# Performance work log

Hardware: AMD Instinct MI355X
Metric: run time of the kernel (lower is better)

## Reference

```python
import jax, jax.numpy as jnp
import numpy as np

N = 100000
E = 6400000
DIMS = [34, 16, 16, 16, 4]


def setup_inputs() -> dict:
    key = jax.random.key(0)
    ks = jax.random.split(key, 12)
    x = jax.random.normal(ks[0], (N, DIMS[0]), dtype=jnp.float32)
    edge_index = jax.random.randint(ks[1], (2, E), 0, N, dtype=jnp.int64)
    inp = {"x": x, "edge_index": edge_index}
    for i in range(4):
        fan_in, fan_out = DIMS[i], DIMS[i + 1]
        s = (6.0 / (fan_in + fan_out)) ** 0.5  # glorot
        inp[f"W{i+1}"] = jax.random.uniform(ks[2 + 2 * i], (fan_in, fan_out), minval=-s, maxval=s, dtype=jnp.float32)
        inp[f"b{i+1}"] = jnp.zeros((fan_out,), dtype=jnp.float32)
    return inp


def gcn_layer(x, W, b, src, dst, norm):
    # x: [N, din] -> [N, dout]; PyG GCNConv: h = XW, aggregate norm*h[src] into dst, + bias
    h = x @ W
    msgs = h[src] * norm[:, None]                      # [E+N, dout]
    out = jax.ops.segment_sum(msgs, dst, num_segments=N)
    return out + b


def reference(x, edge_index, W1, b1, W2, b2, W3, b3, W4, b4):
    loop = jnp.arange(N, dtype=edge_index.dtype)
    src = jnp.concatenate([edge_index[0], loop])       # add self-loops
    dst = jnp.concatenate([edge_index[1], loop])
    deg = jax.ops.segment_sum(jnp.ones_like(dst, dtype=x.dtype), dst, num_segments=N)
    dinv = jnp.where(deg > 0, jax.lax.rsqrt(deg), 0.0)
    norm = dinv[src] * dinv[dst]                       # symmetric normalization per edge
    h = gcn_layer(x, W1, b1, src, dst, norm)
    h = jax.nn.relu(h)
    h = gcn_layer(h, W2, b2, src, dst, norm)
    h = jax.nn.relu(h)
    h = gcn_layer(h, W3, b3, src, dst, norm)
    h = jax.nn.relu(h)
    return gcn_layer(h, W4, b4, src, dst, norm)
```

## Files before the change

kernel.cpp:

```cpp
#include <hip/hip_runtime.h>
#include <hip/hip_bf16.h>


static constexpr int THREADS = 256;
static constexpr int BSHIFT  = 8;
static constexpr int NPB     = 256;
static constexpr int MAXB    = 512;
static constexpr int NCHUNK  = 512;
static constexpr int EPT     = 8;
static constexpr int SSHIFT  = 15;
static constexpr int NSHARD  = 4;


__global__ __launch_bounds__(THREADS)
void k_hist(const int* __restrict__ dst, int* __restrict__ hist_part,
            int e, int nbkt, int chunk) {
    __shared__ int h[MAXB];
    for (int t = threadIdx.x; t < nbkt; t += THREADS) h[t] = 0;
    __syncthreads();
    int beg = blockIdx.x * chunk;
    int end = min(e, beg + chunk);
    for (int base = beg; base < end; base += THREADS * EPT) {
        int i = base + (int)threadIdx.x * EPT;
        if (i + EPT <= end) {
            int4 d0 = *(const int4*)(dst + i);
            int4 d1 = *(const int4*)(dst + i + 4);
            atomicAdd(&h[d0.x >> BSHIFT], 1);
            atomicAdd(&h[d0.y >> BSHIFT], 1);
            atomicAdd(&h[d0.z >> BSHIFT], 1);
            atomicAdd(&h[d0.w >> BSHIFT], 1);
            atomicAdd(&h[d1.x >> BSHIFT], 1);
            atomicAdd(&h[d1.y >> BSHIFT], 1);
            atomicAdd(&h[d1.z >> BSHIFT], 1);
            atomicAdd(&h[d1.w >> BSHIFT], 1);
        } else {
            for (int k = i; k < end; k++) atomicAdd(&h[dst[k] >> BSHIFT], 1);
        }
    }
    __syncthreads();
    for (int t = threadIdx.x; t < nbkt; t += THREADS)
        hist_part[(size_t)blockIdx.x * nbkt + t] = h[t];
}

__global__ __launch_bounds__(NCHUNK)
void k_colscan(int* __restrict__ hist_part, int* __restrict__ btot, int nbkt) {
    __shared__ int s[NCHUNK];
    int b = blockIdx.x;
    int v = hist_part[(size_t)threadIdx.x * nbkt + b];
    s[threadIdx.x] = v;
    __syncthreads();
    for (int ofs = 1; ofs < NCHUNK; ofs <<= 1) {
        int t = (threadIdx.x >= ofs) ? s[threadIdx.x - ofs] : 0;
        __syncthreads();
        s[threadIdx.x] += t;
        __syncthreads();
    }
    hist_part[(size_t)threadIdx.x * nbkt + b] = s[threadIdx.x] - v;
    if (threadIdx.x == NCHUNK - 1) btot[b] = s[NCHUNK - 1];
}

__global__ __launch_bounds__(1024)
void k_scan_b(const int* __restrict__ btot, int* __restrict__ bbase,
              int nbkt, int e) {
    __shared__ int s[1024];
    int v = (threadIdx.x < nbkt) ? btot[threadIdx.x] : 0;
    s[threadIdx.x] = v;
    __syncthreads();
    for (int ofs = 1; ofs < 1024; ofs <<= 1) {
        int t = (threadIdx.x >= ofs) ? s[threadIdx.x - ofs] : 0;
        __syncthreads();
        s[threadIdx.x] += t;
        __syncthreads();
    }
    if (threadIdx.x < nbkt) bbase[threadIdx.x] = s[threadIdx.x] - v;
    if (threadIdx.x == 0) bbase[nbkt] = e;
}

__global__ __launch_bounds__(THREADS)
void k_scatter_bkt(const int* __restrict__ src, const int* __restrict__ dst,
                   const int* __restrict__ offs_part, const int* __restrict__ bbase,
                   int* __restrict__ gpack, int e, int nbkt, int chunk) {
    __shared__ int curs[MAXB];
    for (int t = threadIdx.x; t < nbkt; t += THREADS)
        curs[t] = bbase[t] + offs_part[(size_t)blockIdx.x * nbkt + t];
    __syncthreads();
    int beg = blockIdx.x * chunk;
    int end = min(e, beg + chunk);
    for (int base = beg; base < end; base += THREADS * EPT) {
        int i = base + (int)threadIdx.x * EPT;
        if (i + EPT <= end) {
            int4 s0 = *(const int4*)(src + i);
            int4 s1 = *(const int4*)(src + i + 4);
            int4 d0 = *(const int4*)(dst + i);
            int4 d1 = *(const int4*)(dst + i + 4);
            int p0 = atomicAdd(&curs[d0.x >> BSHIFT], 1);
            int p1 = atomicAdd(&curs[d0.y >> BSHIFT], 1);
            int p2 = atomicAdd(&curs[d0.z >> BSHIFT], 1);
            int p3 = atomicAdd(&curs[d0.w >> BSHIFT], 1);
            int p4 = atomicAdd(&curs[d1.x >> BSHIFT], 1);
            int p5 = atomicAdd(&curs[d1.y >> BSHIFT], 1);
            int p6 = atomicAdd(&curs[d1.z >> BSHIFT], 1);
            int p7 = atomicAdd(&curs[d1.w >> BSHIFT], 1);
            gpack[p0] = (s0.x << BSHIFT) | (d0.x & (NPB - 1));
            gpack[p1] = (s0.y << BSHIFT) | (d0.y & (NPB - 1));
            gpack[p2] = (s0.z << BSHIFT) | (d0.z & (NPB - 1));
            gpack[p3] = (s0.w << BSHIFT) | (d0.w & (NPB - 1));
            gpack[p4] = (s1.x << BSHIFT) | (d1.x & (NPB - 1));
            gpack[p5] = (s1.y << BSHIFT) | (d1.y & (NPB - 1));
            gpack[p6] = (s1.z << BSHIFT) | (d1.z & (NPB - 1));
            gpack[p7] = (s1.w << BSHIFT) | (d1.w & (NPB - 1));
        } else {
            for (int k = i; k < end; k++) {
                int d = dst[k];
                int p = atomicAdd(&curs[d >> BSHIFT], 1);
                gpack[p] = (src[k] << BSHIFT) | (d & (NPB - 1));
            }
        }
    }
}

__global__ __launch_bounds__(THREADS)
void k_bucket_build2(const int* __restrict__ gpack, const int* __restrict__ bbase,
                     int* __restrict__ rowptr2, float* __restrict__ dinv,
                     int* __restrict__ csr, int n, int nbkt) {
    __shared__ int hist2[NPB * NSHARD];
    __shared__ int offs2[NPB * NSHARD];
    __shared__ int scn[THREADS];
    int b = blockIdx.x;
    int node0 = b << BSHIFT;
    int nnodes = min(NPB, n - node0);
    int ebeg = bbase[b];
    int eend = bbase[b + 1];
    int tid = threadIdx.x;

    #pragma unroll
    for (int k = 0; k < NSHARD; k++) hist2[tid * NSHARD + k] = 0;
    __syncthreads();
    for (int i = ebeg + tid; i < eend; i += THREADS) {
        int g = gpack[i];
        int key = (g & (NPB - 1)) * NSHARD + ((g >> BSHIFT) >> SSHIFT);
        atomicAdd(&hist2[key], 1);
    }
    __syncthreads();
    int v0 = hist2[tid * NSHARD + 0];
    int v1 = hist2[tid * NSHARD + 1];
    int v2 = hist2[tid * NSHARD + 2];
    int v3 = hist2[tid * NSHARD + 3];
    int tsum = v0 + v1 + v2 + v3;
    scn[tid] = tsum;
    __syncthreads();
    for (int ofs = 1; ofs < THREADS; ofs <<= 1) {
        int t = (tid >= ofs) ? scn[tid - ofs] : 0;
        __syncthreads();
        scn[tid] += t;
        __syncthreads();
    }
    int excl = scn[tid] - tsum;
    int o0 = excl, o1 = excl + v0, o2 = excl + v0 + v1, o3 = excl + v0 + v1 + v2;
    if (tid < nnodes) {
        int nd = node0 + tid;
        rowptr2[(size_t)nd * NSHARD + 0] = ebeg + o0;
        rowptr2[(size_t)nd * NSHARD + 1] = ebeg + o1;
        rowptr2[(size_t)nd * NSHARD + 2] = ebeg + o2;
        rowptr2[(size_t)nd * NSHARD + 3] = ebeg + o3;
        dinv[nd] = 1.0f / sqrtf((float)(tsum + 1));
    }
    if (b == nbkt - 1 && tid == 0) rowptr2[(size_t)n * NSHARD] = eend;
    offs2[tid * NSHARD + 0] = ebeg + o0;
    offs2[tid * NSHARD + 1] = ebeg + o1;
    offs2[tid * NSHARD + 2] = ebeg + o2;
    offs2[tid * NSHARD + 3] = ebeg + o3;
    __syncthreads();
    for (int i = ebeg + tid; i < eend; i += THREADS) {
        int g = gpack[i];
        int src = g >> BSHIFT;
        int key = (g & (NPB - 1)) * NSHARD + (src >> SSHIFT);
        int pos = atomicAdd(&offs2[key], 1);
        csr[pos] = src;
    }
}


__global__ __launch_bounds__(THREADS)
void k_layer_in(const float* __restrict__ x, const float* __restrict__ W,
                const float* __restrict__ dinv, float* __restrict__ hp, int n) {
    __shared__ float sW[34 * 16];
    for (int t = threadIdx.x; t < 34 * 16; t += THREADS) sW[t] = W[t];
    __syncthreads();
    int i = blockIdx.x * THREADS + threadIdx.x;
    if (i >= n) return;
    float di = dinv[i];
    float acc[16];
    #pragma unroll
    for (int j = 0; j < 16; j++) acc[j] = 0.0f;
    const float* xi = x + (size_t)i * 34;
    #pragma unroll
    for (int k = 0; k < 34; k++) {
        float xk = xi[k];
        #pragma unroll
        for (int j = 0; j < 16; j++) acc[j] = fmaf(xk, sW[k * 16 + j], acc[j]);
    }
    float4* o = (float4*)(hp + (size_t)i * 16);
    o[0] = make_float4(acc[0] * di, acc[1] * di, acc[2] * di, acc[3] * di);
    o[1] = make_float4(acc[4] * di, acc[5] * di, acc[6] * di, acc[7] * di);
    o[2] = make_float4(acc[8] * di, acc[9] * di, acc[10] * di, acc[11] * di);
    o[3] = make_float4(acc[12] * di, acc[13] * di, acc[14] * di, acc[15] * di);
}

__global__ __launch_bounds__(THREADS)
void k_layer_mid2(const float* __restrict__ part, const float* __restrict__ W,
                  const float* __restrict__ bprev, const float* __restrict__ dinv,
                  float* __restrict__ hp, int n) {
    __shared__ float sW[16 * 16];
    __shared__ float sB[16];
    for (int t = threadIdx.x; t < 16 * 16; t += THREADS) sW[t] = W[t];
    if (threadIdx.x < 16) sB[threadIdx.x] = bprev[threadIdx.x];
    __syncthreads();
    int i = blockIdx.x * THREADS + threadIdx.x;
    if (i >= n) return;
    float di = dinv[i];
    size_t stride = (size_t)n * 4;
    const float4* p = (const float4*)(part + (size_t)i * 16);
    float4 a0 = p[0], a1 = p[1], a2 = p[2], a3 = p[3];
    #pragma unroll
    for (int s = 1; s < NSHARD; s++) {
        float4 q0 = p[s * stride + 0], q1 = p[s * stride + 1];
        float4 q2 = p[s * stride + 2], q3 = p[s * stride + 3];
        a0.x += q0.x; a0.y += q0.y; a0.z += q0.z; a0.w += q0.w;
        a1.x += q1.x; a1.y += q1.y; a1.z += q1.z; a1.w += q1.w;
        a2.x += q2.x; a2.y += q2.y; a2.z += q2.z; a2.w += q2.w;
        a3.x += q3.x; a3.y += q3.y; a3.z += q3.z; a3.w += q3.w;
    }
    float xin[16] = {a0.x, a0.y, a0.z, a0.w, a1.x, a1.y, a1.z, a1.w,
                     a2.x, a2.y, a2.z, a2.w, a3.x, a3.y, a3.z, a3.w};
    #pragma unroll
    for (int k = 0; k < 16; k++)
        xin[k] = fmaxf(fmaf(di, xin[k], sB[k]), 0.0f);
    float acc[16];
    #pragma unroll
    for (int j = 0; j < 16; j++) acc[j] = 0.0f;
    #pragma unroll
    for (int k = 0; k < 16; k++) {
        float xk = xin[k];
        #pragma unroll
        for (int j = 0; j < 16; j++) acc[j] = fmaf(xk, sW[k * 16 + j], acc[j]);
    }
    float4* o = (float4*)(hp + (size_t)i * 16);
    o[0] = make_float4(acc[0] * di, acc[1] * di, acc[2] * di, acc[3] * di);
    o[1] = make_float4(acc[4] * di, acc[5] * di, acc[6] * di, acc[7] * di);
    o[2] = make_float4(acc[8] * di, acc[9] * di, acc[10] * di, acc[11] * di);
    o[3] = make_float4(acc[12] * di, acc[13] * di, acc[14] * di, acc[15] * di);
}

__global__ __launch_bounds__(THREADS)
void k_layer_last2(const float* __restrict__ part, const float* __restrict__ W,
                   const float* __restrict__ bprev, const float* __restrict__ dinv,
                   float* __restrict__ hp4, int n) {
    __shared__ float sW[16 * 4];
    __shared__ float sB[16];
    for (int t = threadIdx.x; t < 16 * 4; t += THREADS) sW[t] = W[t];
    if (threadIdx.x < 16) sB[threadIdx.x] = bprev[threadIdx.x];
    __syncthreads();
    int i = blockIdx.x * THREADS + threadIdx.x;
    if (i >= n) return;
    float di = dinv[i];
    size_t stride = (size_t)n * 4;
    const float4* p = (const float4*)(part + (size_t)i * 16);
    float4 a0 = p[0], a1 = p[1], a2 = p[2], a3 = p[3];
    #pragma unroll
    for (int s = 1; s < NSHARD; s++) {
        float4 q0 = p[s * stride + 0], q1 = p[s * stride + 1];
        float4 q2 = p[s * stride + 2], q3 = p[s * stride + 3];
        a0.x += q0.x; a0.y += q0.y; a0.z += q0.z; a0.w += q0.w;
        a1.x += q1.x; a1.y += q1.y; a1.z += q1.z; a1.w += q1.w;
        a2.x += q2.x; a2.y += q2.y; a2.z += q2.z; a2.w += q2.w;
        a3.x += q3.x; a3.y += q3.y; a3.z += q3.z; a3.w += q3.w;
    }
    float xin[16] = {a0.x, a0.y, a0.z, a0.w, a1.x, a1.y, a1.z, a1.w,
                     a2.x, a2.y, a2.z, a2.w, a3.x, a3.y, a3.z, a3.w};
    #pragma unroll
    for (int k = 0; k < 16; k++)
        xin[k] = fmaxf(fmaf(di, xin[k], sB[k]), 0.0f);
    float acc[4];
    #pragma unroll
    for (int j = 0; j < 4; j++) acc[j] = 0.0f;
    #pragma unroll
    for (int k = 0; k < 16; k++) {
        float xk = xin[k];
        #pragma unroll
        for (int j = 0; j < 4; j++) acc[j] = fmaf(xk, sW[k * 4 + j], acc[j]);
    }
    *(float4*)(hp4 + (size_t)i * 4) =
        make_float4(acc[0] * di, acc[1] * di, acc[2] * di, acc[3] * di);
}


__global__ __launch_bounds__(THREADS, 8)
void k_gather16s(const int* __restrict__ rowptr2, const int* __restrict__ csr,
                 const float* __restrict__ hp, float* __restrict__ part, int n) {
    int shard = blockIdx.x & (NSHARD - 1);
    int rg    = blockIdx.x >> 2;
    int row   = rg * 16 + ((int)threadIdx.x >> 4);
    int lane  = threadIdx.x & 15;
    if (row >= n) return;
    int base = (threadIdx.x & 63) & ~15;

    int beg = rowptr2[(size_t)row * NSHARD + shard];
    int end = rowptr2[(size_t)row * NSHARD + shard + 1];
    int len = end - beg;

    float a0 = ((row >> SSHIFT) == shard) ? hp[(size_t)row * 16 + lane] : 0.0f;
    float a1 = 0.f, a2 = 0.f, a3 = 0.f;

    int s0 = 0, s1 = 0;
    if (len > 0)  s0 = csr[min(beg + lane, end - 1)];
    if (len > 16) s1 = csr[min(beg + 16 + lane, end - 1)];

    {
        int cnt = len;
        #pragma unroll
        for (int k = 0; k < 16; k += 4) {
            int sk0 = __shfl(s0, base + k + 0, 64);
            int sk1 = __shfl(s0, base + k + 1, 64);
            int sk2 = __shfl(s0, base + k + 2, 64);
            int sk3 = __shfl(s0, base + k + 3, 64);
            float v0 = hp[(size_t)sk0 * 16 + lane];
            float v1 = hp[(size_t)sk1 * 16 + lane];
            float v2 = hp[(size_t)sk2 * 16 + lane];
            float v3 = hp[(size_t)sk3 * 16 + lane];
            a0 += (k + 0 < cnt) ? v0 : 0.0f;
            a1 += (k + 1 < cnt) ? v1 : 0.0f;
            a2 += (k + 2 < cnt) ? v2 : 0.0f;
            a3 += (k + 3 < cnt) ? v3 : 0.0f;
        }
    }
    {
        int cnt = len - 16;
        #pragma unroll
        for (int k = 0; k < 16; k += 4) {
            int sk0 = __shfl(s1, base + k + 0, 64);
            int sk1 = __shfl(s1, base + k + 1, 64);
            int sk2 = __shfl(s1, base + k + 2, 64);
            int sk3 = __shfl(s1, base + k + 3, 64);
            float v0 = hp[(size_t)sk0 * 16 + lane];
            float v1 = hp[(size_t)sk1 * 16 + lane];
            float v2 = hp[(size_t)sk2 * 16 + lane];
            float v3 = hp[(size_t)sk3 * 16 + lane];
            a0 += (k + 0 < cnt) ? v0 : 0.0f;
            a1 += (k + 1 < cnt) ? v1 : 0.0f;
            a2 += (k + 2 < cnt) ? v2 : 0.0f;
            a3 += (k + 3 < cnt) ? v3 : 0.0f;
        }
    }
    for (int e = beg + 32; e < end; e += 16) {
        int s = csr[min(e + lane, end - 1)];
        int cnt = end - e;
        #pragma unroll
        for (int k = 0; k < 16; k += 4) {
            int sk0 = __shfl(s, base + k + 0, 64);
            int sk1 = __shfl(s, base + k + 1, 64);
            int sk2 = __shfl(s, base + k + 2, 64);
            int sk3 = __shfl(s, base + k + 3, 64);
            float v0 = hp[(size_t)sk0 * 16 + lane];
            float v1 = hp[(size_t)sk1 * 16 + lane];
            float v2 = hp[(size_t)sk2 * 16 + lane];
            float v3 = hp[(size_t)sk3 * 16 + lane];
            a0 += (k + 0 < cnt) ? v0 : 0.0f;
            a1 += (k + 1 < cnt) ? v1 : 0.0f;
            a2 += (k + 2 < cnt) ? v2 : 0.0f;
            a3 += (k + 3 < cnt) ? v3 : 0.0f;
        }
    }
    part[((size_t)shard * n + row) * 16 + lane] = (a0 + a1) + (a2 + a3);
}

__global__ __launch_bounds__(THREADS, 8)
void k_gather4_final(const int* __restrict__ rowptr2, const int* __restrict__ csr,
                     const float* __restrict__ hp, float* __restrict__ outp,
                     const float* __restrict__ dinv, const float* __restrict__ bias,
                     int n) {
    int tid = blockIdx.x * THREADS + threadIdx.x;
    int row = tid >> 4;
    int sub = threadIdx.x & 15;
    int e4  = sub >> 2;
    int ch  = sub & 3;
    if (row >= n) return;
    int base = (threadIdx.x & 63) & ~15;

    int beg = rowptr2[(size_t)row * NSHARD];
    int end = rowptr2[(size_t)(row + 1) * NSHARD];
    int len = end - beg;

    float a = (e4 == 0) ? hp[(size_t)row * 4 + ch] : 0.0f;

    int s0 = 0, s1 = 0;
    if (len > 0)  s0 = csr[min(beg + sub, end - 1)];
    if (len > 16) s1 = csr[min(beg + 16 + sub, end - 1)];

    {
        int cnt = len;
        #pragma unroll
        for (int k = 0; k < 4; k++) {
            int idx = k * 4 + e4;
            int sk = __shfl(s0, base + idx, 64);
            float v = hp[(size_t)sk * 4 + ch];
            a += (idx < cnt) ? v : 0.0f;
        }
    }
    {
        int cnt = len - 16;
        #pragma unroll
        for (int k = 0; k < 4; k++) {
            int idx = k * 4 + e4;
            int sk = __shfl(s1, base + idx, 64);
            float v = hp[(size_t)sk * 4 + ch];
            a += (idx < cnt) ? v : 0.0f;
        }
    }
    for (int e = beg + 32; e < end; e += 16) {
        int s = csr[min(e + sub, end - 1)];
        int cnt = end - e;
        #pragma unroll
        for (int k = 0; k < 4; k++) {
            int idx = k * 4 + e4;
            int sk = __shfl(s, base + idx, 64);
            float v = hp[(size_t)sk * 4 + ch];
            a += (idx < cnt) ? v : 0.0f;
        }
    }
    a += __shfl_xor(a, 4, 64);
    a += __shfl_xor(a, 8, 64);
    if (e4 == 0) outp[(size_t)row * 4 + ch] = fmaf(dinv[row], a, bias[ch]);
}


__global__ __launch_bounds__(THREADS)
void k_zero(int* __restrict__ p, int n) {
    int i = blockIdx.x * THREADS + threadIdx.x;
    if (i < n) p[i] = 0;
}

__global__ __launch_bounds__(THREADS)
void k_count_deg(const int* __restrict__ dst, int* __restrict__ deg, int e) {
    int i = blockIdx.x * THREADS + threadIdx.x;
    if (i >= e) return;
    atomicAdd(&deg[dst[i]], 1);
}

__global__ __launch_bounds__(THREADS)
void k_dinv(const int* __restrict__ deg, float* __restrict__ dinv, int n) {
    int i = blockIdx.x * THREADS + threadIdx.x;
    if (i < n) dinv[i] = 1.0f / sqrtf((float)(deg[i] + 1));
}

__global__ __launch_bounds__(THREADS)
void k_scan1(const int* __restrict__ deg, int* __restrict__ rowptr,
             int* __restrict__ bsum, int n) {
    __shared__ int s[THREADS];
    int i = blockIdx.x * THREADS + threadIdx.x;
    int v = (i < n) ? deg[i] : 0;
    s[threadIdx.x] = v;
    __syncthreads();
    for (int ofs = 1; ofs < THREADS; ofs <<= 1) {
        int t = (threadIdx.x >= ofs) ? s[threadIdx.x - ofs] : 0;
        __syncthreads();
        s[threadIdx.x] += t;
        __syncthreads();
    }
    if (i < n) rowptr[i] = s[threadIdx.x] - v;
    if (threadIdx.x == THREADS - 1) bsum[blockIdx.x] = s[THREADS - 1];
}

__global__ __launch_bounds__(1024)
void k_scan2(int* __restrict__ bsum, int nb) {
    __shared__ int s[1024];
    int v = (threadIdx.x < nb) ? bsum[threadIdx.x] : 0;
    s[threadIdx.x] = v;
    __syncthreads();
    for (int ofs = 1; ofs < 1024; ofs <<= 1) {
        int t = (threadIdx.x >= ofs) ? s[threadIdx.x - ofs] : 0;
        __syncthreads();
        s[threadIdx.x] += t;
        __syncthreads();
    }
    if (threadIdx.x < nb) bsum[threadIdx.x] = s[threadIdx.x] - v;
}

__global__ __launch_bounds__(THREADS)
void k_scan3(int* __restrict__ rowptr, const int* __restrict__ bsum,
             int* __restrict__ cursor, int n, int e) {
    int i = blockIdx.x * THREADS + threadIdx.x;
    if (i < n) {
        int r = rowptr[i] + bsum[blockIdx.x];
        rowptr[i] = r;
        cursor[i] = r;
    }
    if (i == 0) rowptr[n] = e;
}

__global__ __launch_bounds__(THREADS)
void k_fill_cursor(const int* __restrict__ src, const int* __restrict__ dst,
                   int* __restrict__ cursor, int* __restrict__ csr, int e) {
    int i = blockIdx.x * THREADS + threadIdx.x;
    if (i >= e) return;
    int pos = atomicAdd(&cursor[dst[i]], 1);
    csr[pos] = src[i];
}

template<int DIN, int DOUT, bool TRANSFORM>
__global__ __launch_bounds__(THREADS)
void k_layer(const float* __restrict__ in, const float* __restrict__ W,
             const float* __restrict__ bprev, const float* __restrict__ dinv,
             float* __restrict__ hp, int n) {
    __shared__ float sW[DIN * DOUT];
    for (int t = threadIdx.x; t < DIN * DOUT; t += THREADS) sW[t] = W[t];
    __syncthreads();
    int i = blockIdx.x * THREADS + threadIdx.x;
    if (i >= n) return;
    float di = dinv[i];
    float xin[DIN];
    #pragma unroll
    for (int k = 0; k < DIN; k++) xin[k] = in[(size_t)i * DIN + k];
    if constexpr (TRANSFORM) {
        #pragma unroll
        for (int k = 0; k < DIN; k++)
            xin[k] = fmaxf(fmaf(di, xin[k], bprev[k]), 0.0f);
    }
    float acc[DOUT];
    #pragma unroll
    for (int j = 0; j < DOUT; j++) acc[j] = 0.0f;
    #pragma unroll
    for (int k = 0; k < DIN; k++) {
        float xk = xin[k];
        #pragma unroll
        for (int j = 0; j < DOUT; j++) acc[j] = fmaf(xk, sW[k * DOUT + j], acc[j]);
    }
    #pragma unroll
    for (int j = 0; j < DOUT; j++) hp[(size_t)i * DOUT + j] = acc[j] * di;
}

template<int D, bool FINAL>
__global__ __launch_bounds__(THREADS)
void k_gather(const int* __restrict__ rowptr, const int* __restrict__ csr,
              const float* __restrict__ hp, float* __restrict__ outp,
              const float* __restrict__ dinv, const float* __restrict__ bias,
              int n) {
    int tid  = blockIdx.x * THREADS + threadIdx.x;
    int row  = tid / D;
    int lane = tid & (D - 1);
    if (row >= n) return;
    int base = (threadIdx.x & 63) & ~(D - 1);
    int beg = rowptr[row];
    int end = rowptr[row + 1];
    float a0 = hp[(size_t)row * D + lane];
    float a1 = 0.f, a2 = 0.f, a3 = 0.f;
    int e = beg;
    for (; e + D <= end; e += D) {
        int s = csr[e + lane];
        #pragma unroll
        for (int k = 0; k < D; k += 4) {
            int s0 = __shfl(s, base + k + 0, 64);
            int s1 = __shfl(s, base + k + 1, 64);
            int s2 = __shfl(s, base + k + 2, 64);
            int s3 = __shfl(s, base + k + 3, 64);
            a0 += hp[(size_t)s0 * D + lane];
            a1 += hp[(size_t)s1 * D + lane];
            a2 += hp[(size_t)s2 * D + lane];
            a3 += hp[(size_t)s3 * D + lane];
        }
    }
    if (e < end) {
        int idx = e + lane;
        int s = (idx < end) ? csr[idx] : 0;
        int cnt = end - e;
        for (int k = 0; k < cnt; k++) {
            int sk = __shfl(s, base + k, 64);
            a0 += hp[(size_t)sk * D + lane];
        }
    }
    float acc = (a0 + a1) + (a2 + a3);
    if constexpr (FINAL) {
        outp[(size_t)row * D + lane] = fmaf(dinv[row], acc, bias[lane]);
    } else {
        outp[(size_t)row * D + lane] = acc;
    }
}


extern "C" void kernel_launch(void* const* d_in, const int* in_sizes, int n_in,
                              void* d_out, int out_size, void* d_ws, size_t ws_size,
                              hipStream_t stream) {
    const float* x   = (const float*)d_in[0];
    const int*   ei  = (const int*)d_in[1];
    const float* W1  = (const float*)d_in[2];
    const float* b1  = (const float*)d_in[3];
    const float* W2  = (const float*)d_in[4];
    const float* b2  = (const float*)d_in[5];
    const float* W3  = (const float*)d_in[6];
    const float* b3  = (const float*)d_in[7];
    const float* W4  = (const float*)d_in[8];
    const float* b4  = (const float*)d_in[9];
    float*       out = (float*)d_out;

    const int N = in_sizes[0] / 34;
    const int E = in_sizes[1] / 2;
    const int* src = ei;
    const int* dst = ei + E;

    const int gN  = (N + THREADS - 1) / THREADS;
    const int g4  = (int)(((size_t)N * 4 + THREADS - 1) / THREADS);

    const int nbkt  = (N + NPB - 1) >> BSHIFT;
    const int chunk = (((E + NCHUNK - 1) / NCHUNK) + EPT - 1) & ~(EPT - 1);
    const int gG    = ((N + 15) / 16) * NSHARD;
    const int gF    = (int)(((size_t)N * 16 + THREADS - 1) / THREADS);

    {
        char* ws = (char*)d_ws;
        size_t off = 0;
        auto alloc = [&](size_t bytes) -> void* {
            void* p = ws + off;
            off += (bytes + 255) & ~(size_t)255;
            return p;
        };
        float* dinv    = (float*)alloc((size_t)N * 4);
        float* hp      = (float*)alloc((size_t)N * 16 * 4);
        float* part    = (float*)alloc((size_t)NSHARD * N * 16 * 4);
        float* hp4     = (float*)alloc((size_t)N * 4 * 4);
        int*   rowptr2 = (int*)  alloc(((size_t)N * NSHARD + 1) * 4);
        int*   csr     = (int*)  alloc((size_t)E * 4);
        int*   gpack   = (int*)  alloc((size_t)E * 4);
        int*   offsp   = (int*)  alloc((size_t)NCHUNK * nbkt * 4);
        int*   btot    = (int*)  alloc((size_t)nbkt * 4);
        int*   bbase   = (int*)  alloc((size_t)(nbkt + 1) * 4);

        bool aligned16 = (((uintptr_t)src & 15) == 0) && (((uintptr_t)dst & 15) == 0);
        bool fast_ok = (nbkt <= MAXB) && (off <= ws_size) && aligned16 &&
                       (N <= (1 << (31 - BSHIFT))) &&
                       (N <= (NSHARD << SSHIFT));

        if (fast_ok) {
            k_hist        <<<NCHUNK, THREADS, 0, stream>>>(dst, offsp, E, nbkt, chunk);
            k_colscan     <<<nbkt, NCHUNK, 0, stream>>>(offsp, btot, nbkt);
            k_scan_b      <<<1, 1024, 0, stream>>>(btot, bbase, nbkt, E);
            k_scatter_bkt <<<NCHUNK, THREADS, 0, stream>>>(src, dst, offsp, bbase,
                                                           gpack, E, nbkt, chunk);
            k_bucket_build2<<<nbkt, THREADS, 0, stream>>>(gpack, bbase, rowptr2,
                                                          dinv, csr, N, nbkt);

            k_layer_in <<<gN, THREADS, 0, stream>>>(x, W1, dinv, hp, N);
            k_gather16s<<<gG, THREADS, 0, stream>>>(rowptr2, csr, hp, part, N);

            k_layer_mid2<<<gN, THREADS, 0, stream>>>(part, W2, b1, dinv, hp, N);
            k_gather16s<<<gG, THREADS, 0, stream>>>(rowptr2, csr, hp, part, N);

            k_layer_mid2<<<gN, THREADS, 0, stream>>>(part, W3, b2, dinv, hp, N);
            k_gather16s<<<gG, THREADS, 0, stream>>>(rowptr2, csr, hp, part, N);

            k_layer_last2<<<gN, THREADS, 0, stream>>>(part, W4, b3, dinv, hp4, N);
            k_gather4_final<<<gF, THREADS, 0, stream>>>(rowptr2, csr, hp4, out,
                                                        dinv, b4, N);
            return;
        }
    }

    {
        char* ws = (char*)d_ws;
        size_t off = 0;
        auto alloc = [&](size_t bytes) -> void* {
            void* p = ws + off;
            off += (bytes + 255) & ~(size_t)255;
            return p;
        };
        int*   deg    = (int*)  alloc((size_t)N * 4);
        float* dinv   = (float*)alloc((size_t)N * 4);
        float* bufA   = (float*)alloc((size_t)N * 16 * 4);
        float* bufB   = (float*)alloc((size_t)N * 16 * 4);
        int*   rowptr = (int*)  alloc((size_t)(N + 1) * 4);
        int*   cursor = (int*)  alloc((size_t)N * 4);
        const int nb  = (N + THREADS - 1) / THREADS;
        int*   bsum   = (int*)  alloc((size_t)nb * 4);
        int*   csr    = (int*)  alloc((size_t)E * 4);

        const int gE  = (E + THREADS - 1) / THREADS;
        const int g16 = (int)(((size_t)N * 16 + THREADS - 1) / THREADS);

        k_zero<<<gN, THREADS, 0, stream>>>(deg, N);
        k_count_deg<<<gE, THREADS, 0, stream>>>(dst, deg, E);
        k_dinv<<<gN, THREADS, 0, stream>>>(deg, dinv, N);
        k_scan1<<<nb, THREADS, 0, stream>>>(deg, rowptr, bsum, N);
        k_scan2<<<1, 1024, 0, stream>>>(bsum, nb);
        k_scan3<<<nb, THREADS, 0, stream>>>(rowptr, bsum, cursor, N, E);
        k_fill_cursor<<<gE, THREADS, 0, stream>>>(src, dst, cursor, csr, E);

        k_layer<34, 16, false><<<gN, THREADS, 0, stream>>>(x, W1, nullptr, dinv, bufA, N);
        k_gather<16, false><<<g16, THREADS, 0, stream>>>(rowptr, csr, bufA, bufB, nullptr, nullptr, N);

        k_layer<16, 16, true><<<gN, THREADS, 0, stream>>>(bufB, W2, b1, dinv, bufA, N);
        k_gather<16, false><<<g16, THREADS, 0, stream>>>(rowptr, csr, bufA, bufB, nullptr, nullptr, N);

        k_layer<16, 16, true><<<gN, THREADS, 0, stream>>>(bufB, W3, b2, dinv, bufA, N);
        k_gather<16, false><<<g16, THREADS, 0, stream>>>(rowptr, csr, bufA, bufB, nullptr, nullptr, N);

        k_layer<16, 4, true><<<gN, THREADS, 0, stream>>>(bufB, W4, b3, dinv, bufA, N);
        k_gather<4, true><<<g4, THREADS, 0, stream>>>(rowptr, csr, bufA, out, dinv, b4, N);
    }
}
```

Measured before the change: 340.1 us.

## Split bucket build into rowptr pass and LDS-staged CSR fill with smaller buckets

Halves the node bucket size (128 nodes per bucket, up to 1024 buckets) and cuts histogram chunks from 512 to 128. The old combined build kernel becomes two kernels: one computes rowptr and dinv, and a second scatters sources into an LDS staging buffer, then writes the bucket's CSR slice out contiguously. The staging is meant to turn random global scatter writes into coalesced ones. The cost is an extra kernel launch, a second pass over gpack, and about 40KB of LDS per block, which may limit occupancy.

```diff
diff --git a/kernel.cpp b/kernel.cpp
--- a/kernel.cpp
+++ b/kernel.cpp
@@ -2,14 +2,15 @@
 #include <hip/hip_bf16.h>
 
 
-static constexpr int THREADS = 256;
-static constexpr int BSHIFT  = 8;
-static constexpr int NPB     = 256;
-static constexpr int MAXB    = 512;
-static constexpr int NCHUNK  = 512;
-static constexpr int EPT     = 8;
-static constexpr int SSHIFT  = 15;
-static constexpr int NSHARD  = 4;
+static constexpr int THREADS   = 256;
+static constexpr int BSHIFT    = 7;
+static constexpr int NPB       = 128;
+static constexpr int MAXB      = 1024;
+static constexpr int NCHUNK    = 128;
+static constexpr int EPT       = 8;
+static constexpr int SSHIFT    = 15;
+static constexpr int NSHARD    = 4;
+static constexpr int STAGE_CAP = 10240;
 
 
 __global__ __launch_bounds__(THREADS)
@@ -120,11 +121,10 @@
 }
 
 __global__ __launch_bounds__(THREADS)
-void k_bucket_build2(const int* __restrict__ gpack, const int* __restrict__ bbase,
-                     int* __restrict__ rowptr2, float* __restrict__ dinv,
-                     int* __restrict__ csr, int n, int nbkt) {
+void k_rowptr2(const int* __restrict__ gpack, const int* __restrict__ bbase,
+               int* __restrict__ rowptr2, float* __restrict__ dinv,
+               int n, int nbkt) {
     __shared__ int hist2[NPB * NSHARD];
-    __shared__ int offs2[NPB * NSHARD];
     __shared__ int scn[THREADS];
     int b = blockIdx.x;
     int node0 = b << BSHIFT;
@@ -133,8 +133,7 @@
     int eend = bbase[b + 1];
     int tid = threadIdx.x;
 
-    #pragma unroll
-    for (int k = 0; k < NSHARD; k++) hist2[tid * NSHARD + k] = 0;
+    for (int t = tid; t < NPB * NSHARD; t += THREADS) hist2[t] = 0;
     __syncthreads();
     for (int i = ebeg + tid; i < eend; i += THREADS) {
         int g = gpack[i];
@@ -142,11 +141,14 @@
         atomicAdd(&hist2[key], 1);
     }
     __syncthreads();
-    int v0 = hist2[tid * NSHARD + 0];
-    int v1 = hist2[tid * NSHARD + 1];
-    int v2 = hist2[tid * NSHARD + 2];
-    int v3 = hist2[tid * NSHARD + 3];
-    int tsum = v0 + v1 + v2 + v3;
+    int v0 = 0, v1 = 0, v2 = 0, v3 = 0, tsum = 0;
+    if (tid < NPB) {
+        v0 = hist2[tid * NSHARD + 0];
+        v1 = hist2[tid * NSHARD + 1];
+        v2 = hist2[tid * NSHARD + 2];
+        v3 = hist2[tid * NSHARD + 3];
+        tsum = v0 + v1 + v2 + v3;
+    }
     scn[tid] = tsum;
     __syncthreads();
     for (int ofs = 1; ofs < THREADS; ofs <<= 1) {
@@ -156,27 +158,53 @@
         __syncthreads();
     }
     int excl = scn[tid] - tsum;
-    int o0 = excl, o1 = excl + v0, o2 = excl + v0 + v1, o3 = excl + v0 + v1 + v2;
     if (tid < nnodes) {
         int nd = node0 + tid;
-        rowptr2[(size_t)nd * NSHARD + 0] = ebeg + o0;
-        rowptr2[(size_t)nd * NSHARD + 1] = ebeg + o1;
-        rowptr2[(size_t)nd * NSHARD + 2] = ebeg + o2;
-        rowptr2[(size_t)nd * NSHARD + 3] = ebeg + o3;
+        rowptr2[(size_t)nd * NSHARD + 0] = ebeg + excl;
+        rowptr2[(size_t)nd * NSHARD + 1] = ebeg + excl + v0;
+        rowptr2[(size_t)nd * NSHARD + 2] = ebeg + excl + v0 + v1;
+        rowptr2[(size_t)nd * NSHARD + 3] = ebeg + excl + v0 + v1 + v2;
         dinv[nd] = 1.0f / sqrtf((float)(tsum + 1));
     }
     if (b == nbkt - 1 && tid == 0) rowptr2[(size_t)n * NSHARD] = eend;
-    offs2[tid * NSHARD + 0] = ebeg + o0;
-    offs2[tid * NSHARD + 1] = ebeg + o1;
-    offs2[tid * NSHARD + 2] = ebeg + o2;
-    offs2[tid * NSHARD + 3] = ebeg + o3;
-    __syncthreads();
-    for (int i = ebeg + tid; i < eend; i += THREADS) {
-        int g = gpack[i];
-        int src = g >> BSHIFT;
-        int key = (g & (NPB - 1)) * NSHARD + (src >> SSHIFT);
-        int pos = atomicAdd(&offs2[key], 1);
-        csr[pos] = src;
+}
+
+__global__ __launch_bounds__(THREADS)
+void k_fill_staged(const int* __restrict__ gpack, const int* __restrict__ bbase,
+                   const int* __restrict__ rowptr2, int* __restrict__ csr,
+                   int n, int nbkt) {
+    __shared__ int curs[NPB * NSHARD];
+    __shared__ int staged[STAGE_CAP];
+    int b = blockIdx.x;
+    int node0 = b << BSHIFT;
+    int tid = threadIdx.x;
+    int ebeg = bbase[b];
+    int eend = bbase[b + 1];
+    int len = eend - ebeg;
+
+    for (int t = tid; t < NPB * NSHARD; t += THREADS) {
+        int nd = node0 + (t >> 2);
+        curs[t] = (nd < n) ? rowptr2[(size_t)nd * NSHARD + (t & 3)] : 0;
+    }
+    __syncthreads();
+
+    if (len <= STAGE_CAP) {
+        for (int i = ebeg + tid; i < eend; i += THREADS) {
+            int g = gpack[i];
+            int key = (g & (NPB - 1)) * NSHARD + ((g >> BSHIFT) >> SSHIFT);
+            int pos = atomicAdd(&curs[key], 1);
+            staged[pos - ebeg] = g >> BSHIFT;
+        }
+        __syncthreads();
+        for (int i = tid; i < len; i += THREADS)
+            csr[ebeg + i] = staged[i];
+    } else {
+        for (int i = ebeg + tid; i < eend; i += THREADS) {
+            int g = gpack[i];
+            int key = (g & (NPB - 1)) * NSHARD + ((g >> BSHIFT) >> SSHIFT);
+            int pos = atomicAdd(&curs[key], 1);
+            csr[pos] = g >> BSHIFT;
+        }
     }
 }
 
@@ -608,7 +636,6 @@
     const int* dst = ei + E;
 
     const int gN  = (N + THREADS - 1) / THREADS;
-    const int g4  = (int)(((size_t)N * 4 + THREADS - 1) / THREADS);
 
     const int nbkt  = (N + NPB - 1) >> BSHIFT;
     const int chunk = (((E + NCHUNK - 1) / NCHUNK) + EPT - 1) & ~(EPT - 1);
@@ -636,7 +663,7 @@
 
         bool aligned16 = (((uintptr_t)src & 15) == 0) && (((uintptr_t)dst & 15) == 0);
         bool fast_ok = (nbkt <= MAXB) && (off <= ws_size) && aligned16 &&
-                       (N <= (1 << (31 - BSHIFT))) &&
+                       (N <= (1 << (31 - BSHIFT - 1))) &&
                        (N <= (NSHARD << SSHIFT));
 
         if (fast_ok) {
@@ -645,8 +672,10 @@
             k_scan_b      <<<1, 1024, 0, stream>>>(btot, bbase, nbkt, E);
             k_scatter_bkt <<<NCHUNK, THREADS, 0, stream>>>(src, dst, offsp, bbase,
                                                            gpack, E, nbkt, chunk);
-            k_bucket_build2<<<nbkt, THREADS, 0, stream>>>(gpack, bbase, rowptr2,
-                                                          dinv, csr, N, nbkt);
+            k_rowptr2     <<<nbkt, THREADS, 0, stream>>>(gpack, bbase, rowptr2,
+                                                         dinv, N, nbkt);
+            k_fill_staged <<<nbkt, THREADS, 0, stream>>>(gpack, bbase, rowptr2,
+                                                         csr, N, nbkt);
 
             k_layer_in <<<gN, THREADS, 0, stream>>>(x, W1, dinv, hp, N);
             k_gather16s<<<gG, THREADS, 0, stream>>>(rowptr2, csr, hp, part, N);
@@ -684,6 +713,7 @@
 
         const int gE  = (E + THREADS - 1) / THREADS;
         const int g16 = (int)(((size_t)N * 16 + THREADS - 1) / THREADS);
+        const int g4  = (int)(((size_t)N * 4 + THREADS - 1) / THREADS);
 
         k_zero<<<gN, THREADS, 0, stream>>>(deg, N);
         k_count_deg<<<gE, THREADS, 0, stream>>>(dst, deg, E);
```

After: 315.0 us. 7.4% less time.
